# Kernel tuning notes

Hardware: AMD Instinct MI355X
Metric: run time of the kernel (lower is better)

Reference implementation:

```python
import jax, jax.numpy as jnp
import numpy as np

AR_COEF = 0.01
TAR_COEF = 0.01
LN_EPS = 1e-5


def setup_inputs() -> dict:
    key = jax.random.key(0)
    ks = jax.random.split(key, 8)
    B, T, D, E, H, A = 32, 512, 256, 1024, 1024, 64
    def rn(k, shape, fan_in):
        return jax.random.normal(k, shape, jnp.float32) * (1.0 / np.sqrt(fan_in))
    return {
        "obs": jax.random.normal(ks[0], (B, T, D), jnp.float32),
        "hxs": jnp.zeros((B, H), jnp.float32),
        "cxs": jnp.zeros((B, H), jnp.float32),
        "W1": rn(ks[1], (E, D), D), "b1": jnp.zeros((E,), jnp.float32),
        "W2": rn(ks[2], (E, E), E), "b2": jnp.zeros((E,), jnp.float32),
        "W_ih": rn(ks[3], (4 * H, E), E),
        "W_hh": rn(ks[4], (4 * H, H), H),
        "b_ih": jnp.zeros((4 * H,), jnp.float32),
        "b_hh": jnp.zeros((4 * H,), jnp.float32),
        "ln_g": jnp.ones((H,), jnp.float32), "ln_b": jnp.zeros((H,), jnp.float32),
        "Wa": rn(ks[5], (A, H), H), "ba": jnp.zeros((A,), jnp.float32),
        "Wc": rn(ks[6], (1, H), H), "bc": jnp.zeros((1,), jnp.float32),
    }


def reference(obs, hxs, cxs, W1, b1, W2, b2, W_ih, W_hh, b_ih, b_hh,
              ln_g, ln_b, Wa, ba, Wc, bc):
    # obs encoder (identity) + 2-layer SiLU MLP encoder
    enc = jax.nn.silu(obs @ W1.T + b1)        # (B,T,E)
    enc = jax.nn.silu(enc @ W2.T + b2)        # (B,T,E)

    # precompute input-to-gate contributions; gates in PyTorch order i,f,g,o
    x_gates = enc @ W_ih.T + (b_ih + b_hh)    # (B,T,4H)
    xg = jnp.transpose(x_gates, (1, 0, 2))    # (T,B,4H)

    def step(carry, xt):
        h, c = carry
        g = xt + h @ W_hh.T                   # (B,4H)
        i, f, gg, o = jnp.split(g, 4, axis=-1)
        c = jax.nn.sigmoid(f) * c + jax.nn.sigmoid(i) * jnp.tanh(gg)
        h = jax.nn.sigmoid(o) * jnp.tanh(c)
        return (h, c), h

    (h_n, c_n), outs = jax.lax.scan(step, (hxs, cxs), xg)
    out = jnp.transpose(outs, (1, 0, 2))      # (B,T,H)

    # LayerNorm
    mu = out.mean(-1, keepdims=True)
    var = ((out - mu) ** 2).mean(-1, keepdims=True)
    out_ln = (out - mu) * jax.lax.rsqrt(var + LN_EPS) * ln_g + ln_b

    ar_loss = (out_ln ** 2).mean() * AR_COEF
    tar_loss = ((out_ln[:, 1:, :] - out_ln[:, :-1, :]) ** 2).mean() * TAR_COEF

    logits = out_ln @ Wa.T + ba               # (B,T,A)
    values = (out_ln @ Wc.T + bc)[..., 0]     # (B,T)
    return logits, values, h_n, c_n, ar_loss, tar_loss
```

## Files before the change

### kernel.cpp

```cpp
#include <hip/hip_runtime.h>

typedef __attribute__((ext_vector_type(8))) short bf16x8;
typedef __attribute__((ext_vector_type(8))) unsigned short u16x8;
typedef __attribute__((ext_vector_type(4))) unsigned short u16x4;
typedef __attribute__((ext_vector_type(4))) float f32x4;
typedef __attribute__((ext_vector_type(2))) unsigned int u32x2;

#define NB 32
#define NT 512
#define ND 256
#define NE 1024
#define NH 1024
#define LSTM_SMEM (131072 + 18432)

__device__ __forceinline__ float bf2f(unsigned short u){
  union { unsigned int i; float f; } w; w.i = ((unsigned int)u) << 16; return w.f;
}
__device__ __forceinline__ unsigned short f2bf(float f){
  union { float f; unsigned int i; } w; w.f = f;
  unsigned int r = (w.i >> 16) & 1u;
  return (unsigned short)((w.i + 0x7fffu + r) >> 16);
}

__device__ __forceinline__ bf16x8 bypass_load_b128(const unsigned short* p){
  bf16x8 r;
  asm volatile("global_load_dwordx4 %0, %1, off sc0 sc1" : "=v"(r) : "v"(p) : "memory");
  return r;
}
__device__ __forceinline__ int bypass_load_i32(const int* p){
  int r;
  asm volatile("global_load_dword %0, %1, off sc0 sc1\n\ts_waitcnt vmcnt(0)"
               : "=v"(r) : "v"(p) : "memory");
  return r;
}
__device__ __forceinline__ void bypass_store_b64(unsigned short* p, u32x2 v){
  asm volatile("global_store_dwordx2 %0, %1, off sc0 sc1" :: "v"(p), "v"(v) : "memory");
}
__device__ __forceinline__ void bypass_store_i32(int* p, int v){
  asm volatile("global_store_dword %0, %1, off sc0 sc1" :: "v"(p), "v"(v) : "memory");
}

__device__ __forceinline__ void gload_lds16(const void* g, void* l){
  __builtin_amdgcn_global_load_lds(
      (const __attribute__((address_space(1))) void*)g,
      (__attribute__((address_space(3))) void*)l, 16, 0, 0);
}

__global__ void mega_prep(const float* __restrict__ W1, const float* __restrict__ W2,
                          const float* __restrict__ Wih,
                          const float* __restrict__ Wa, const float* __restrict__ Wc,
                          const float* __restrict__ ba, const float* __restrict__ bc,
                          const float* __restrict__ b_ih, const float* __restrict__ b_hh,
                          const float* __restrict__ hxs, const float* __restrict__ cxs,
                          unsigned short* __restrict__ W1_b, unsigned short* __restrict__ W2_b,
                          unsigned short* __restrict__ Wih_b, unsigned short* __restrict__ Whead_b,
                          float* __restrict__ bias_heads, float* __restrict__ bias_xg,
                          unsigned short* __restrict__ h16, float* __restrict__ c_buf,
                          int* __restrict__ flags)
{
  long i0 = (long)blockIdx.x*256 + threadIdx.x;
  long stride = (long)gridDim.x*256;
  for (long i=i0; i<(long)NE*ND;   i+=stride) W1_b[i]  = f2bf(W1[i]);
  for (long i=i0; i<(long)NE*NE;   i+=stride) W2_b[i]  = f2bf(W2[i]);
  for (long i=i0; i<(long)4*NH*NE; i+=stride) Wih_b[i] = f2bf(Wih[i]);
  for (long i=i0; i<128*1024; i+=stride){
    int n = (int)(i>>10), k = (int)(i&1023);
    Whead_b[i] = f2bf(n<64 ? Wa[i] : (n==64 ? Wc[k] : 0.f));
  }
  for (long i=i0; i<4096; i+=stride) bias_xg[i] = b_ih[i] + b_hh[i];
  for (long i=i0; i<65;   i+=stride) bias_heads[i] = (i<64) ? ba[i] : bc[0];
  for (long i=i0; i<NB*NH; i+=stride){ h16[i] = f2bf(hxs[i]); c_buf[i] = cxs[i]; }
  for (long i=i0; i<8192; i+=stride) flags[i] = 0;
}

__global__ void f2b_obs_chunk(const float* __restrict__ obs, unsigned short* __restrict__ dst,
                              int lgTc, int t0){
  const int Tc = 1 << lgTc;
  const long n = (long)NB * Tc * ND;
  long i = (long)blockIdx.x*blockDim.x + threadIdx.x;
  long stride = (long)gridDim.x*blockDim.x;
  for (; i < n; i += stride){
    long lr = i >> 8;
    int col = (int)(i & 255);
    long gr = (lr >> lgTc)*NT + t0 + (lr & (Tc-1));
    dst[i] = f2bf(obs[gr*ND + col]);
  }
}

__global__ void sentinel_kernel(float* __restrict__ out){ out[0] = 1.0e6f; }

#define GEMM_COMPUTE(P) { \
  bf16x8 af[4], bfr[4]; \
  _Pragma("unroll") for (int f=0; f<4; f++){ \
    af[f]  = *(const bf16x8*)&As[P][(wm*64 + f*16 + fr)*32 + kf]; \
    bfr[f] = *(const bf16x8*)&Bs[P][(wn*64 + f*16 + fr)*32 + kf]; } \
  _Pragma("unroll") for (int i=0;i<4;i++) \
    _Pragma("unroll") for (int j=0;j<4;j++) \
      acc[i][j] = __builtin_amdgcn_mfma_f32_16x16x32_bf16(af[i], bfr[j], acc[i][j], 0, 0, 0); }

template<int SILU, int HEADS>
__global__ __launch_bounds__(256)
void gemm_bt(const unsigned short* __restrict__ A, const unsigned short* __restrict__ Bw,
             const float* __restrict__ bias, unsigned short* __restrict__ C,
             float* __restrict__ oLogits, float* __restrict__ oValues,
             int K, int N, int Nreal)
{
  __shared__ __align__(16) unsigned short As[2][128*32];
  __shared__ __align__(16) unsigned short Bs[2][128*32];
  const int tid = threadIdx.x;
  const int lane = tid & 63;
  const int w = tid >> 6;
  const int wm = w >> 1, wn = w & 1;
  const int m0 = blockIdx.x * 128, n0 = blockIdx.y * 128;
  f32x4 acc[4][4];
#pragma unroll
  for (int i=0;i<4;i++)
#pragma unroll
    for (int j=0;j<4;j++){ f32x4 z = {0.f,0.f,0.f,0.f}; acc[i][j] = z; }
  const int fr = lane & 15;
  const int kf = (lane >> 4) * 8;
  const int r0 = tid >> 2, s0 = tid & 3;
  const unsigned short* gA0 = A  + (size_t)(m0+r0)*K    + s0*8;
  const unsigned short* gA1 = A  + (size_t)(m0+r0+64)*K + s0*8;
  const unsigned short* gB0 = Bw + (size_t)(n0+r0)*K    + s0*8;
  const unsigned short* gB1 = Bw + (size_t)(n0+r0+64)*K + s0*8;

  auto stage = [&](int p, int k0){
    char* a = (char*)&As[p][0] + w*1024;
    char* b = (char*)&Bs[p][0] + w*1024;
    gload_lds16(gA0 + k0, a);
    gload_lds16(gA1 + k0, a + 4096);
    gload_lds16(gB0 + k0, b);
    gload_lds16(gB1 + k0, b + 4096);
  };

  stage(0, 0);
  asm volatile("s_waitcnt vmcnt(0)" ::: "memory");
  __syncthreads();
  int cur = 0;
  for (int k0 = 32; k0 < K; k0 += 32){
    stage(cur ^ 1, k0);
    GEMM_COMPUTE(cur);
    asm volatile("s_waitcnt vmcnt(0)" ::: "memory");
    __syncthreads();
    cur ^= 1;
  }
  GEMM_COMPUTE(cur);

  const int mb = (lane >> 4) * 4;
  const int nb = lane & 15;
#pragma unroll
  for (int i=0;i<4;i++)
#pragma unroll
    for (int j=0;j<4;j++)
#pragma unroll
      for (int r=0;r<4;r++){
        int m = m0 + wm*64 + i*16 + mb + r;
        int n = n0 + wn*64 + j*16 + nb;
        if (HEADS && n >= Nreal) continue;
        float v = acc[i][j][r] + bias[n];
        if (SILU) v = v / (1.f + expf(-v));
        if (!HEADS) {
          C[(size_t)m*N + n] = f2bf(v);
        } else {
          if (n < 64) oLogits[(size_t)m*64 + n] = v;
          else if (n == 64) oValues[m] = v;
        }
      }
}

__global__ __launch_bounds__(512)
void lstm_mfma(const unsigned short* __restrict__ xg, const float* __restrict__ Whh,
               unsigned short* __restrict__ h16, float* __restrict__ c_buf,
               unsigned short* __restrict__ hist, float* __restrict__ dh, float* __restrict__ dc,
               int* __restrict__ flags, int t0, int t1, int Tc)
{
  extern __shared__ char smem[];
  unsigned short* Wf = (unsigned short*)smem;
  float* red = (float*)(smem + 131072);
  const int wg = blockIdx.x;
  const int bh = wg & 1, ug = wg >> 1;
  const int b0 = bh*16, n0w = ug*8;
  const int tid = threadIdx.x;
  const int lane = tid & 63;
  const int wv = tid >> 6;
  const int fr = lane & 15;
  const int q8 = (lane >> 4) * 8;

  for (int s = tid; s < 8192; s += 512){
    int term = s >> 12, kt = (s >> 7) & 31, nt = (s >> 6) & 1, l = s & 63;
    int r = nt*16 + (l & 15);
    int g = r >> 3, uu2 = r & 7;
    const float* src = Whh + (size_t)(g*NH + n0w + uu2)*NH + kt*32 + (l>>4)*8;
    u16x8 o;
#pragma unroll
    for (int j=0;j<8;j++){
      float wv_ = src[j];
      unsigned short hi = f2bf(wv_);
      o[j] = (term==0) ? hi : f2bf(wv_ - bf2f(hi));
    }
    *(u16x8*)&Wf[(size_t)s*8] = o;
  }

  const int bl = wv*2 + (lane >> 3);
  const int uu = lane & 7;
  float c_reg = 0.f, h_keep = 0.f;
  if (lane < 16) c_reg = c_buf[(b0 + bl)*NH + n0w + uu];
  __syncthreads();

  int pcur = t0 % 3;
  for (int t = t0; t < t1; t++){
    const int pnext = (pcur == 2) ? 0 : pcur + 1;
    const unsigned short* hb = h16 + (size_t)pcur  * (NB*NH);
    unsigned short* hb_next  = h16 + (size_t)pnext * (NB*NH);
    const int tl = t - t0;

    float xgv[4] = {0.f,0.f,0.f,0.f};
    if (lane < 16){
      size_t xbase = ((size_t)(b0+bl)*Tc + tl)*4096 + n0w + uu;
#pragma unroll
      for (int g=0; g<4; g++) xgv[g] = bf2f(xg[xbase + g*1024]);
    }

    {
      const int pw = ((wv*16 + fr)*2 + bh) * 32;
      while (true){
        int v = bypass_load_i32(&flags[pw]);
        v = min(v, __shfl_xor(v, 1));
        v = min(v, __shfl_xor(v, 2));
        v = min(v, __shfl_xor(v, 4));
        v = min(v, __shfl_xor(v, 8));
        if (v >= t) break;
        __builtin_amdgcn_s_sleep(1);
      }
    }

    bf16x8 a[4];
#pragma unroll
    for (int ks=0; ks<4; ks++)
      a[ks] = bypass_load_b128(hb + (size_t)(b0 + fr)*NH + (wv*4 + ks)*32 + q8);
    asm volatile("s_waitcnt vmcnt(0)" ::: "memory");
    __builtin_amdgcn_sched_barrier(0);

    f32x4 acc[2];
    { f32x4 z = {0.f,0.f,0.f,0.f}; acc[0] = z; acc[1] = z; }
#pragma unroll
    for (int ks=0; ks<4; ks++){
      int kt = wv*4 + ks;
#pragma unroll
      for (int nt=0; nt<2; nt++){
        bf16x8 bhi = *(const bf16x8*)&Wf[kt*1024 + nt*512 + lane*8];
        bf16x8 blo = *(const bf16x8*)&Wf[32768 + kt*1024 + nt*512 + lane*8];
        acc[nt] = __builtin_amdgcn_mfma_f32_16x16x32_bf16(a[ks], bhi, acc[nt], 0,0,0);
        acc[nt] = __builtin_amdgcn_mfma_f32_16x16x32_bf16(a[ks], blo, acc[nt], 0,0,0);
      }
    }

#pragma unroll
    for (int nt=0; nt<2; nt++)
#pragma unroll
      for (int r4=0; r4<4; r4++){
        int batch = (lane>>4)*4 + r4;
        red[batch*288 + (nt*16 + fr)*9 + wv] = acc[nt][r4];
      }
    __syncthreads();

    if (lane < 16){
      float gate[4];
#pragma unroll
      for (int g=0; g<4; g++){
        const float* rp = &red[bl*288 + (g*8 + uu)*9];
        float s = 0.f;
#pragma unroll
        for (int w8=0; w8<8; w8++) s += rp[w8];
        gate[g] = s + xgv[g];
      }
      float iv = 1.f/(1.f+expf(-gate[0]));
      float fv = 1.f/(1.f+expf(-gate[1]));
      float gv = tanhf(gate[2]);
      float ov = 1.f/(1.f+expf(-gate[3]));
      float c_new = fv*c_reg + iv*gv;
      float h_new = ov*tanhf(c_new);
      c_reg = c_new; h_keep = h_new;
      float h0 = __shfl(h_new, (lane & ~3) + 0);
      float h1 = __shfl(h_new, (lane & ~3) + 1);
      float h2 = __shfl(h_new, (lane & ~3) + 2);
      float h3 = __shfl(h_new, (lane & ~3) + 3);
      if ((lane & 3) == 0){
        unsigned short p0 = f2bf(h0), p1 = f2bf(h1), p2 = f2bf(h2), p3 = f2bf(h3);
        u32x2 pk; pk[0] = (unsigned)p0 | ((unsigned)p1 << 16);
        pk[1] = (unsigned)p2 | ((unsigned)p3 << 16);
        bypass_store_b64(hb_next + (size_t)(b0+bl)*NH + n0w + uu, pk);
        u16x4 hp = { p0, p1, p2, p3 };
        *(u16x4*)&hist[((size_t)(b0+bl)*Tc + tl)*NH + n0w + uu] = hp;
      }
    }
    asm volatile("s_waitcnt vmcnt(0)" ::: "memory");
    __syncthreads();
    if (tid == 0) bypass_store_i32(&flags[wg*32], t+1);
    pcur = pnext;
  }
  if (lane < 16){
    c_buf[(b0+bl)*NH + n0w + uu] = c_reg;
    if (t1 == NT){ dh[(b0+bl)*NH + n0w + uu] = h_keep; dc[(b0+bl)*NH + n0w + uu] = c_reg; }
  }
}

__global__ __launch_bounds__(256)
void ln_chunk(const unsigned short* __restrict__ X, const float* __restrict__ gam, const float* __restrict__ bet,
              unsigned short* __restrict__ Y, int lgTc, int t0)
{
  const int Tc = 1 << lgTc;
  const int row = blockIdx.x*4 + (threadIdx.x >> 6);
  const int lane = threadIdx.x & 63;
  const int bl = row >> lgTc, tl = row & (Tc-1);
  const long grow = (long)bl*NT + t0 + tl;
  u16x8 a0 = *(const u16x8*)&X[(size_t)row*NH + lane*16];
  u16x8 a1 = *(const u16x8*)&X[(size_t)row*NH + lane*16 + 8];
  float x[16];
  float s = 0.f;
#pragma unroll
  for (int j=0;j<8;j++){ x[j] = bf2f(a0[j]); x[8+j] = bf2f(a1[j]); }
#pragma unroll
  for (int j=0;j<16;j++) s += x[j];
  s += __shfl_xor(s,1); s += __shfl_xor(s,2); s += __shfl_xor(s,4);
  s += __shfl_xor(s,8); s += __shfl_xor(s,16); s += __shfl_xor(s,32);
  const float mean = s * (1.0f/NH);
  float q = 0.f;
#pragma unroll
  for (int j=0;j<16;j++){ float d = x[j]-mean; q += d*d; }
  q += __shfl_xor(q,1); q += __shfl_xor(q,2); q += __shfl_xor(q,4);
  q += __shfl_xor(q,8); q += __shfl_xor(q,16); q += __shfl_xor(q,32);
  const float rs = 1.f / sqrtf(q * (1.0f/NH) + 1e-5f);
  f32x4 g0 = *(const f32x4*)&gam[lane*16];
  f32x4 g1 = *(const f32x4*)&gam[lane*16+4];
  f32x4 g2 = *(const f32x4*)&gam[lane*16+8];
  f32x4 g3 = *(const f32x4*)&gam[lane*16+12];
  f32x4 b0 = *(const f32x4*)&bet[lane*16];
  f32x4 b1 = *(const f32x4*)&bet[lane*16+4];
  f32x4 b2 = *(const f32x4*)&bet[lane*16+8];
  f32x4 b3 = *(const f32x4*)&bet[lane*16+12];
  u16x8 o0, o1;
#pragma unroll
  for (int j=0;j<4;j++){
    o0[j]   = f2bf((x[j]   -mean)*rs*g0[j] + b0[j]);
    o0[4+j] = f2bf((x[4+j] -mean)*rs*g1[j] + b1[j]);
    o1[j]   = f2bf((x[8+j] -mean)*rs*g2[j] + b2[j]);
    o1[4+j] = f2bf((x[12+j]-mean)*rs*g3[j] + b3[j]);
  }
  *(u16x8*)&Y[(size_t)grow*NH + lane*16]     = o0;
  *(u16x8*)&Y[(size_t)grow*NH + lane*16 + 8] = o1;
}

__global__ __launch_bounds__(256)
void loss_partial(const unsigned short* __restrict__ Yu, float* __restrict__ partials)
{
  float ar = 0.f, tar = 0.f;
  long stride = (long)gridDim.x*256;
  for (long vv = (long)blockIdx.x*256 + threadIdx.x; vv < 2097152; vv += stride){
    long i = vv*8;
    int t = (int)((i >> 10) & 511);
    u16x8 y = *(const u16x8*)&Yu[i];
    float x[8];
#pragma unroll
    for (int q=0;q<8;q++){ x[q] = bf2f(y[q]); ar += x[q]*x[q]; }
    if (t > 0){
      u16x8 yp = *(const u16x8*)&Yu[i - 1024];
#pragma unroll
      for (int q=0;q<8;q++){ float d = x[q] - bf2f(yp[q]); tar += d*d; }
    }
  }
  ar += __shfl_xor(ar,1); ar += __shfl_xor(ar,2); ar += __shfl_xor(ar,4);
  ar += __shfl_xor(ar,8); ar += __shfl_xor(ar,16); ar += __shfl_xor(ar,32);
  tar += __shfl_xor(tar,1); tar += __shfl_xor(tar,2); tar += __shfl_xor(tar,4);
  tar += __shfl_xor(tar,8); tar += __shfl_xor(tar,16); tar += __shfl_xor(tar,32);
  __shared__ float red[16];
  int w = threadIdx.x >> 6;
  if ((threadIdx.x & 63) == 0){ red[w] = ar; red[8+w] = tar; }
  __syncthreads();
  if (threadIdx.x == 0){
    partials[blockIdx.x*2]   = red[0]+red[1]+red[2]+red[3];
    partials[blockIdx.x*2+1] = red[8]+red[9]+red[10]+red[11];
  }
}

__global__ __launch_bounds__(256)
void loss_final(const float* __restrict__ partials, float* __restrict__ oAr, float* __restrict__ oTar){
  double sa = 0.0, st = 0.0;
  for (int i = threadIdx.x; i < 1024; i += 256){ sa += (double)partials[2*i]; st += (double)partials[2*i+1]; }
  for (int m=1;m<64;m<<=1){ sa += __shfl_xor(sa, m); st += __shfl_xor(st, m); }
  __shared__ double rd[8];
  int w = threadIdx.x >> 6;
  if ((threadIdx.x & 63) == 0){ rd[w] = sa; rd[4+w] = st; }
  __syncthreads();
  if (threadIdx.x == 0){
    double a  = rd[0]+rd[1]+rd[2]+rd[3];
    double tt = rd[4]+rd[5]+rd[6]+rd[7];
    oAr[0]  = (float)(a  / 16777216.0 * 0.01);
    oTar[0] = (float)(tt / 16744448.0 * 0.01);
  }
}

extern "C" void kernel_launch(void* const* d_in, const int* in_sizes, int n_in,
                              void* d_out, int out_size, void* d_ws, size_t ws_size,
                              hipStream_t stream)
{
  const float* obs  = (const float*)d_in[0];
  const float* hxs  = (const float*)d_in[1];
  const float* cxs  = (const float*)d_in[2];
  const float* W1   = (const float*)d_in[3];
  const float* b1   = (const float*)d_in[4];
  const float* W2   = (const float*)d_in[5];
  const float* b2   = (const float*)d_in[6];
  const float* W_ih = (const float*)d_in[7];
  const float* W_hh = (const float*)d_in[8];
  const float* b_ih = (const float*)d_in[9];
  const float* b_hh = (const float*)d_in[10];
  const float* ln_g = (const float*)d_in[11];
  const float* ln_b = (const float*)d_in[12];
  const float* Wa   = (const float*)d_in[13];
  const float* ba   = (const float*)d_in[14];
  const float* Wc   = (const float*)d_in[15];
  const float* bc   = (const float*)d_in[16];

  char* ws = (char*)d_ws;
  size_t off = 0;
  auto alloc = [&](size_t bytes)->char*{
    char* p = ws + off;
    off = (off + bytes + 255) & ~(size_t)255;
    return p;
  };
  unsigned short* W1_b    = (unsigned short*)alloc((size_t)NE*ND*2);
  unsigned short* W2_b    = (unsigned short*)alloc((size_t)NE*NE*2);
  unsigned short* Wih_b   = (unsigned short*)alloc((size_t)4*NH*NE*2);
  unsigned short* Whead_b = (unsigned short*)alloc((size_t)128*NH*2);
  float* bias_heads       = (float*)alloc(65*4);
  float* bias_xg          = (float*)alloc(4096*4);
  unsigned short* outln_b = (unsigned short*)alloc((size_t)NB*NT*NH*2);
  unsigned short* h16     = (unsigned short*)alloc((size_t)3*NB*NH*2);
  float* c_buf            = (float*)alloc((size_t)NB*NH*4);
  int*   flags            = (int*)alloc(8192*4);
  float* partials         = (float*)alloc((size_t)1024*2*4);
  const size_t fixedEnd = off;

  int lg = -1;
  for (int L = 9; L >= 4; --L){
    size_t Mc = (size_t)NB << L;
    size_t per = Mc*ND*2 + 2*(Mc*NE*2) + Mc*4096*2 + Mc*NH*2 + 6*256;
    if (fixedEnd + per <= ws_size){ lg = L; break; }
  }
  if (lg < 0){ sentinel_kernel<<<1,1,0,stream>>>((float*)d_out); return; }
  const int Tc = 1 << lg;
  const int Mc = NB << lg;
  const int nChunks = NT >> lg;

  unsigned short* obs_c  = (unsigned short*)alloc((size_t)Mc*ND*2);
  unsigned short* enc1_c = (unsigned short*)alloc((size_t)Mc*NE*2);
  unsigned short* enc2_c = (unsigned short*)alloc((size_t)Mc*NE*2);
  unsigned short* xg_c   = (unsigned short*)alloc((size_t)Mc*4096*2);
  unsigned short* hist_c = (unsigned short*)alloc((size_t)Mc*NH*2);

  float* o = (float*)d_out;
  float* oLogits = o;
  float* oValues = o + (size_t)NB*NT*64;
  float* oH  = oValues + NB*NT;
  float* oC  = oH + NB*NH;
  float* oAr = oC + NB*NH;
  float* oTar= oAr + 1;

  mega_prep<<<2048,256,0,stream>>>(W1, W2, W_ih, Wa, Wc, ba, bc, b_ih, b_hh, hxs, cxs,
                                   W1_b, W2_b, Wih_b, Whead_b, bias_heads, bias_xg,
                                   h16, c_buf, flags);

  for (int c = 0; c < nChunks; ++c){
    int t0 = c << lg, t1 = t0 + Tc;
    f2b_obs_chunk<<<512,256,0,stream>>>(obs, obs_c, lg, t0);
    gemm_bt<1,0><<<dim3(Mc/128,8) ,256,0,stream>>>(obs_c,  W1_b,  b1,      enc1_c, nullptr, nullptr, ND, NE, NE);
    gemm_bt<1,0><<<dim3(Mc/128,8) ,256,0,stream>>>(enc1_c, W2_b,  b2,      enc2_c, nullptr, nullptr, NE, NE, NE);
    gemm_bt<0,0><<<dim3(Mc/128,32),256,0,stream>>>(enc2_c, Wih_b, bias_xg, xg_c,   nullptr, nullptr, NE, 4096, 4096);

    lstm_mfma<<<256,512,LSTM_SMEM,stream>>>(xg_c, W_hh, h16, c_buf, hist_c, oH, oC, flags, t0, t1, Tc);

    ln_chunk<<<Mc/4,256,0,stream>>>(hist_c, ln_g, ln_b, outln_b, lg, t0);
  }

  gemm_bt<0,1><<<dim3(128,1),256,0,stream>>>(outln_b, Whead_b, bias_heads, nullptr, oLogits, oValues, NH, 128, 65);
  loss_partial<<<1024,256,0,stream>>>(outln_b, partials);
  loss_final<<<1,256,0,stream>>>(partials, oAr, oTar);
}
```

Measured before the change: 2.213 ms.

## Swizzle GEMM block order, stream xg stores, defer LSTM history store past flag

Remaps GEMM block indices into an XCD-aware order, so blocks sharing an N tile and neighbouring M tiles land on the same die and reuse cached weights. The xg projection output is written with cache-bypassing short stores, so the LSTM reads it coherently and it does not pollute cache. In the LSTM step, the history write moves after the s_waitcnt and flag publish, taking it off the critical synchronisation path between timesteps. Per-element bypass short stores may be less efficient than normal cached writes.

```diff
diff --git a/kernel.cpp b/kernel.cpp
--- a/kernel.cpp
+++ b/kernel.cpp
@@ -38,6 +38,9 @@
 }
 __device__ __forceinline__ void bypass_store_i32(int* p, int v){
   asm volatile("global_store_dword %0, %1, off sc0 sc1" :: "v"(p), "v"(v) : "memory");
+}
+__device__ __forceinline__ void bypass_store_u16(unsigned short* p, unsigned short v){
+  asm volatile("global_store_short %0, %1, off sc0 sc1" :: "v"(p), "v"(v) : "memory");
 }
 
 __device__ __forceinline__ void gload_lds16(const void* g, void* l){
@@ -98,7 +101,7 @@
     _Pragma("unroll") for (int j=0;j<4;j++) \
       acc[i][j] = __builtin_amdgcn_mfma_f32_16x16x32_bf16(af[i], bfr[j], acc[i][j], 0, 0, 0); }
 
-template<int SILU, int HEADS>
+template<int SILU, int HEADS, int STREAMC>
 __global__ __launch_bounds__(256)
 void gemm_bt(const unsigned short* __restrict__ A, const unsigned short* __restrict__ Bw,
              const float* __restrict__ bias, unsigned short* __restrict__ C,
@@ -111,7 +114,17 @@
   const int lane = tid & 63;
   const int w = tid >> 6;
   const int wm = w >> 1, wn = w & 1;
-  const int m0 = blockIdx.x * 128, n0 = blockIdx.y * 128;
+  const int gx = gridDim.x;
+  const int jf = blockIdx.y * gx + blockIdx.x;
+  int m0, n0;
+  if ((gx & 7) == 0){
+    const int ms = gx >> 3;
+    const int x = jf & 7, ii = jf >> 3;
+    m0 = (x*ms + (ii % ms)) * 128;
+    n0 = (ii / ms) * 128;
+  } else {
+    m0 = blockIdx.x * 128; n0 = blockIdx.y * 128;
+  }
   f32x4 acc[4][4];
 #pragma unroll
   for (int i=0;i<4;i++)
@@ -161,7 +174,9 @@
         float v = acc[i][j][r] + bias[n];
         if (SILU) v = v / (1.f + expf(-v));
         if (!HEADS) {
-          C[(size_t)m*N + n] = f2bf(v);
+          unsigned short cv = f2bf(v);
+          if (STREAMC) bypass_store_u16(&C[(size_t)m*N + n], cv);
+          else         C[(size_t)m*N + n] = cv;
         } else {
           if (n < 64) oLogits[(size_t)m*64 + n] = v;
           else if (n == 64) oValues[m] = v;
@@ -265,6 +280,7 @@
       }
     __syncthreads();
 
+    unsigned short p0=0,p1=0,p2=0,p3=0;
     if (lane < 16){
       float gate[4];
 #pragma unroll
@@ -287,17 +303,19 @@
       float h2 = __shfl(h_new, (lane & ~3) + 2);
       float h3 = __shfl(h_new, (lane & ~3) + 3);
       if ((lane & 3) == 0){
-        unsigned short p0 = f2bf(h0), p1 = f2bf(h1), p2 = f2bf(h2), p3 = f2bf(h3);
+        p0 = f2bf(h0); p1 = f2bf(h1); p2 = f2bf(h2); p3 = f2bf(h3);
         u32x2 pk; pk[0] = (unsigned)p0 | ((unsigned)p1 << 16);
         pk[1] = (unsigned)p2 | ((unsigned)p3 << 16);
         bypass_store_b64(hb_next + (size_t)(b0+bl)*NH + n0w + uu, pk);
-        u16x4 hp = { p0, p1, p2, p3 };
-        *(u16x4*)&hist[((size_t)(b0+bl)*Tc + tl)*NH + n0w + uu] = hp;
       }
     }
     asm volatile("s_waitcnt vmcnt(0)" ::: "memory");
     __syncthreads();
     if (tid == 0) bypass_store_i32(&flags[wg*32], t+1);
+    if (lane < 16 && (lane & 3) == 0){
+      u16x4 hp = { p0, p1, p2, p3 };
+      *(u16x4*)&hist[((size_t)(b0+bl)*Tc + tl)*NH + n0w + uu] = hp;
+    }
     pcur = pnext;
   }
   if (lane < 16){
@@ -475,16 +493,16 @@
   for (int c = 0; c < nChunks; ++c){
     int t0 = c << lg, t1 = t0 + Tc;
     f2b_obs_chunk<<<512,256,0,stream>>>(obs, obs_c, lg, t0);
-    gemm_bt<1,0><<<dim3(Mc/128,8) ,256,0,stream>>>(obs_c,  W1_b,  b1,      enc1_c, nullptr, nullptr, ND, NE, NE);
-    gemm_bt<1,0><<<dim3(Mc/128,8) ,256,0,stream>>>(enc1_c, W2_b,  b2,      enc2_c, nullptr, nullptr, NE, NE, NE);
-    gemm_bt<0,0><<<dim3(Mc/128,32),256,0,stream>>>(enc2_c, Wih_b, bias_xg, xg_c,   nullptr, nullptr, NE, 4096, 4096);
+    gemm_bt<1,0,0><<<dim3(Mc/128,8) ,256,0,stream>>>(obs_c,  W1_b,  b1,      enc1_c, nullptr, nullptr, ND, NE, NE);
+    gemm_bt<1,0,0><<<dim3(Mc/128,8) ,256,0,stream>>>(enc1_c, W2_b,  b2,      enc2_c, nullptr, nullptr, NE, NE, NE);
+    gemm_bt<0,0,1><<<dim3(Mc/128,32),256,0,stream>>>(enc2_c, Wih_b, bias_xg, xg_c,   nullptr, nullptr, NE, 4096, 4096);
 
     lstm_mfma<<<256,512,LSTM_SMEM,stream>>>(xg_c, W_hh, h16, c_buf, hist_c, oH, oC, flags, t0, t1, Tc);
 
     ln_chunk<<<Mc/4,256,0,stream>>>(hist_c, ln_g, ln_b, outln_b, lg, t0);
   }
 
-  gemm_bt<0,1><<<dim3(128,1),256,0,stream>>>(outln_b, Whead_b, bias_heads, nullptr, oLogits, oValues, NH, 128, 65);
+  gemm_bt<0,1,0><<<dim3(128,1),256,0,stream>>>(outln_b, Whead_b, bias_heads, nullptr, oLogits, oValues, NH, 128, 65);
   loss_partial<<<1024,256,0,stream>>>(outln_b, partials);
   loss_final<<<1,256,0,stream>>>(partials, oAr, oTar);
 }
```

New measurement: 2.260 ms. 1.02x slower.
